# Optimization experiments

Measured on AMD Instinct MI355X. Metric: run time of the kernel, lower is better.

Reference implementation:

```python
import jax, jax.numpy as jnp
import numpy as np

IGNORE_INDEX = -100
VOCAB = 32000
D_MODEL = 2048


def setup_inputs() -> dict:
    key = jax.random.key(0)
    k1, k2, k3 = jax.random.split(key, 3)
    outputs = jax.random.normal(k1, (4, 2048, D_MODEL), dtype=jnp.float32)
    targets = jax.random.randint(k2, (4, 2048), 0, VOCAB, dtype=jnp.int64)
    # LM-head projection weight (torch nn.Linear stores [out_features, in_features]; no bias for LM heads)
    weight = jax.random.normal(k3, (VOCAB, D_MODEL), dtype=jnp.float32) * (D_MODEL ** -0.5)
    return {"outputs": outputs, "targets": targets, "weight": weight}


def reference(outputs, targets, weight):
    # Flatten tokens: [B, S, D] -> [N, D], [B, S] -> [N]
    d = outputs.shape[-1]
    hidden = outputs.reshape(-1, d)
    tgt = targets.reshape(-1)
    valid = tgt != IGNORE_INDEX
    safe_tgt = jnp.where(valid, tgt, 0)

    # Linear projection fused conceptually with CE; per-chunk sum-reduction CE
    # summed over chunks equals the full-batch sum, so we compute it vectorized.
    logits = jnp.einsum("nd,vd->nv", hidden, weight).astype(jnp.float32)  # [N, V]
    logp = jax.nn.log_softmax(logits, axis=-1)
    nll = -jnp.take_along_axis(logp, safe_tgt[:, None], axis=-1)[:, 0]  # [N]

    total_valid = jnp.sum(valid)
    total_loss = jnp.sum(jnp.where(valid, nll, 0.0))
    # forward returns 0.0 when no valid tokens; guard the division
    return jnp.where(total_valid > 0, total_loss / jnp.maximum(total_valid, 1).astype(total_loss.dtype), 0.0)
```

## Files before the change

### kernel.cpp

```cpp
#include <hip/hip_runtime.h>
#include <hip/hip_bf16.h>
#include <math.h>

#define D_MODEL 2048
#define VOCAB   32000
#define NTOK    8192
#define NCHUNK  (VOCAB / 64)

#define BM      128
#define BN      128
#define BK      32
#define LDK     (BK + 8)
#define MTILES  (NTOK / BM)
#define NTILES  (VOCAB / BN)

#define BM2     256
#define BN2     256
#define SUBK    64
#define NSUB    (D_MODEL / SUBK)
#define SUBSZ   32768
#define MT2     (NTOK / BM2)
#define NT2     (VOCAB / BN2)

typedef __attribute__((ext_vector_type(8))) short  frag8;
typedef __attribute__((ext_vector_type(4))) float  f32x4;
typedef __attribute__((ext_vector_type(4))) int    i32x4;
typedef __attribute__((ext_vector_type(8))) int    i32x8;


__device__ inline void g2l16(const void* g, void* l) {
    __builtin_amdgcn_global_load_lds(
        (const __attribute__((address_space(1))) unsigned int*)g,
        (__attribute__((address_space(3))) unsigned int*)l,
        16, 0, 0);
}

__device__ inline unsigned pack_bf16(float x, float y) {
    union { float f; unsigned u; } a, b;
    a.f = x; b.f = y;
    return __builtin_amdgcn_perm(b.u, a.u, 0x07060302u);
}


__global__ void cvt_fp8_kernel(const float* __restrict__ src, unsigned char* __restrict__ dst) {
    size_t i = (size_t)blockIdx.x * 256 + threadIdx.x;
    float4 v0 = ((const float4*)src)[2 * i];
    float4 v1 = ((const float4*)src)[2 * i + 1];
    int lo = 0, hi = 0;
    lo = __builtin_amdgcn_cvt_pk_fp8_f32(v0.x, v0.y, lo, 0);
    lo = __builtin_amdgcn_cvt_pk_fp8_f32(v0.z, v0.w, lo, 1);
    hi = __builtin_amdgcn_cvt_pk_fp8_f32(v1.x, v1.y, hi, 0);
    hi = __builtin_amdgcn_cvt_pk_fp8_f32(v1.z, v1.w, hi, 1);
    uint2 o = { (unsigned)lo, (unsigned)hi };
    ((uint2*)dst)[i] = o;
}


__global__ __launch_bounds__(512, 2)
void gemm_lse_fp8_v2(const unsigned char* __restrict__ Hq, const unsigned char* __restrict__ Wq,
                     float* __restrict__ partials) {
    extern __shared__ unsigned char lds[];

    const int L  = (blockIdx.x & 7) * 500 + (blockIdx.x >> 3);
    const int qs = L / 1000;
    const int rs = L % 1000;
    const int mtile = (rs & 7) + qs * 8;
    const int ntile = (rs >> 3) % 125;
    const int m0 = mtile * BM2;
    const int n0 = ntile * BN2;

    const int tid  = threadIdx.x;
    const int lane = tid & 63;
    const int w    = tid >> 6;
    const int wr   = w >> 2;
    const int wc   = w & 3;
    const int q    = lane >> 4;
    const int c    = lane & 15;

    const int sline = tid >> 3;
    const int sp    = (tid & 7) ^ (sline & 7);
    const int srow  = 2 * sline + (sp >> 2);
    const int sjj   = sp & 3;
    const unsigned char* gA = Hq + (size_t)(m0 + srow) * D_MODEL + sjj * 16;
    const unsigned char* gB = Wq + (size_t)(n0 + srow) * D_MODEL + sjj * 16;
    const unsigned wbase = (unsigned)w * 1024;

    const int prow = c >> 1;
    const int qh   = q >> 1;
    const int qb   = q & 1;
    const unsigned sA    = (unsigned)((((c & 1) << 2) | (qb << 1)) ^ prow) << 4;
    const unsigned aoff0 = (unsigned)(wr * 64 + prow) * 128 + sA;
    const unsigned aoff1 = aoff0 ^ 16;
    const unsigned boff0 = 16384u + (unsigned)(wc * 32 + prow) * 128 + sA;
    const unsigned boff1 = boff0 ^ 16;

    f32x4 acc[8][4];
    const f32x4 zero = {0.f, 0.f, 0.f, 0.f};
    #pragma unroll
    for (int i = 0; i < 8; ++i)
        #pragma unroll
        for (int j = 0; j < 4; ++j) acc[i][j] = zero;

    auto STAGE = [&](int s) {
        const unsigned base = (unsigned)(s & 3) * (unsigned)SUBSZ;
        const size_t ko = (size_t)s * SUBK;
        g2l16(gA + ko,                           lds + base + wbase);
        g2l16(gA + ko + (size_t)128 * D_MODEL,   lds + base + 8192 + wbase);
        g2l16(gB + ko,                           lds + base + 16384 + wbase);
        g2l16(gB + ko + (size_t)128 * D_MODEL,   lds + base + 24576 + wbase);
    };

    STAGE(0); STAGE(1); STAGE(2); STAGE(3);

    union Frag { i32x8 v; i32x4 h[2]; };

    #pragma unroll 1
    for (int t = 0; t < 16; ++t) {
        if (t == 15) asm volatile("s_waitcnt vmcnt(0)" ::: "memory");
        else         asm volatile("s_waitcnt vmcnt(8)" ::: "memory");
        __builtin_amdgcn_s_barrier();

        const unsigned ring   = (unsigned)(t & 1) * (2u * SUBSZ);
        const unsigned subsel = ring + (unsigned)qh * SUBSZ;
        const unsigned char* a0 = lds + subsel + aoff0;
        const unsigned char* a1 = lds + subsel + aoff1;
        const unsigned char* b0 = lds + subsel + boff0;
        const unsigned char* b1 = lds + subsel + boff1;

        i32x8 b8[4], fa, fb;

        #pragma unroll
        for (int ni = 0; ni < 4; ++ni) {
            Frag f;
            f.h[0] = *(const i32x4*)(b0 + ni * 1024);
            f.h[1] = *(const i32x4*)(b1 + ni * 1024);
            b8[ni] = f.v;
        }
        {
            Frag f0, f1;
            f0.h[0] = *(const i32x4*)(a0 + 0 * 1024);
            f0.h[1] = *(const i32x4*)(a1 + 0 * 1024);
            f1.h[0] = *(const i32x4*)(a0 + 1 * 1024);
            f1.h[1] = *(const i32x4*)(a1 + 1 * 1024);
            fa = f0.v; fb = f1.v;
        }
        asm volatile("s_waitcnt lgkmcnt(8)" ::: "memory");
        __builtin_amdgcn_s_barrier();
        asm volatile("s_waitcnt lgkmcnt(0)" ::: "memory");
        __builtin_amdgcn_sched_barrier(0);
        __builtin_amdgcn_s_setprio(1);
        #pragma unroll
        for (int ni = 0; ni < 4; ++ni)
            acc[0][ni] = __builtin_amdgcn_mfma_scale_f32_16x16x128_f8f6f4(
                fa, b8[ni], acc[0][ni], 0, 0, 0, 0x7F7F7F7F, 0, 0x7F7F7F7F);
        #pragma unroll
        for (int ni = 0; ni < 4; ++ni)
            acc[1][ni] = __builtin_amdgcn_mfma_scale_f32_16x16x128_f8f6f4(
                fb, b8[ni], acc[1][ni], 0, 0, 0, 0x7F7F7F7F, 0, 0x7F7F7F7F);
        __builtin_amdgcn_s_setprio(0);
        __builtin_amdgcn_s_barrier();

        #pragma unroll
        for (int p = 1; p < 3; ++p) {
            Frag f0, f1;
            f0.h[0] = *(const i32x4*)(a0 + (2 * p) * 1024);
            f0.h[1] = *(const i32x4*)(a1 + (2 * p) * 1024);
            f1.h[0] = *(const i32x4*)(a0 + (2 * p + 1) * 1024);
            f1.h[1] = *(const i32x4*)(a1 + (2 * p + 1) * 1024);
            fa = f0.v; fb = f1.v;
            __builtin_amdgcn_s_barrier();
            asm volatile("s_waitcnt lgkmcnt(0)" ::: "memory");
            __builtin_amdgcn_sched_barrier(0);
            __builtin_amdgcn_s_setprio(1);
            #pragma unroll
            for (int ni = 0; ni < 4; ++ni)
                acc[2 * p][ni] = __builtin_amdgcn_mfma_scale_f32_16x16x128_f8f6f4(
                    fa, b8[ni], acc[2 * p][ni], 0, 0, 0, 0x7F7F7F7F, 0, 0x7F7F7F7F);
            #pragma unroll
            for (int ni = 0; ni < 4; ++ni)
                acc[2 * p + 1][ni] = __builtin_amdgcn_mfma_scale_f32_16x16x128_f8f6f4(
                    fb, b8[ni], acc[2 * p + 1][ni], 0, 0, 0, 0x7F7F7F7F, 0, 0x7F7F7F7F);
            __builtin_amdgcn_s_setprio(0);
            __builtin_amdgcn_s_barrier();
        }

        {
            Frag f0, f1;
            f0.h[0] = *(const i32x4*)(a0 + 6 * 1024);
            f0.h[1] = *(const i32x4*)(a1 + 6 * 1024);
            f1.h[0] = *(const i32x4*)(a0 + 7 * 1024);
            f1.h[1] = *(const i32x4*)(a1 + 7 * 1024);
            fa = f0.v; fb = f1.v;
        }
        asm volatile("s_waitcnt lgkmcnt(0)" ::: "memory");
        __builtin_amdgcn_s_barrier();
        __builtin_amdgcn_sched_barrier(0);
        if (t < 14) { STAGE(2 * t + 4); STAGE(2 * t + 5); }
        __builtin_amdgcn_sched_barrier(0);
        __builtin_amdgcn_s_setprio(1);
        #pragma unroll
        for (int ni = 0; ni < 4; ++ni)
            acc[6][ni] = __builtin_amdgcn_mfma_scale_f32_16x16x128_f8f6f4(
                fa, b8[ni], acc[6][ni], 0, 0, 0, 0x7F7F7F7F, 0, 0x7F7F7F7F);
        #pragma unroll
        for (int ni = 0; ni < 4; ++ni)
            acc[7][ni] = __builtin_amdgcn_mfma_scale_f32_16x16x128_f8f6f4(
                fb, b8[ni], acc[7][ni], 0, 0, 0, 0x7F7F7F7F, 0, 0x7F7F7F7F);
        __builtin_amdgcn_s_setprio(0);
    }

    const int chunk = ntile * 4 + wc;
    #pragma unroll
    for (int mi = 0; mi < 8; ++mi) {
        #pragma unroll
        for (int r = 0; r < 4; ++r) {
            float v0 = acc[mi][0][r], v1 = acc[mi][1][r];
            float v2 = acc[mi][2][r], v3 = acc[mi][3][r];
            float mx = fmaxf(fmaxf(v0, v1), fmaxf(v2, v3));
            #pragma unroll
            for (int mask = 1; mask <= 8; mask <<= 1)
                mx = fmaxf(mx, __shfl_xor(mx, mask, 64));
            float sm = __expf(v0 - mx) + __expf(v1 - mx)
                     + __expf(v2 - mx) + __expf(v3 - mx);
            #pragma unroll
            for (int mask = 1; mask <= 8; mask <<= 1)
                sm += __shfl_xor(sm, mask, 64);
            if (c == 0) {
                int row_g = m0 + wr * 128 + mi * 16 + q * 4 + r;
                float* p = partials + ((size_t)row_g * NCHUNK + chunk) * 2;
                p[0] = mx;
                p[1] = sm;
            }
        }
    }
}


__global__ __launch_bounds__(256, 2)
void gemm_lse_f32(const float* __restrict__ H, const float* __restrict__ W,
                  float* __restrict__ partials) {
    __shared__ unsigned short As[BM][LDK];
    __shared__ unsigned short Bs[BN][LDK];

    const int GM = 8;
    int bid   = blockIdx.x;
    int super = bid / (GM * NTILES);
    int rem   = bid % (GM * NTILES);
    int mtile = super * GM + (rem % GM);
    int ntile = rem / GM;

    const int m0 = mtile * BM;
    const int n0 = ntile * BN;

    const int tid  = threadIdx.x;
    const int lane = tid & 63;
    const int w    = tid >> 6;
    const int wm   = (w >> 1) * 64;
    const int wn   = (w & 1)  * 64;
    const int q    = lane >> 4;
    const int c    = lane & 15;

    f32x4 acc[4][4];
    const f32x4 zero = {0.f, 0.f, 0.f, 0.f};
    #pragma unroll
    for (int i = 0; i < 4; ++i)
        #pragma unroll
        for (int j = 0; j < 4; ++j) acc[i][j] = zero;

    for (int kt = 0; kt < D_MODEL / BK; ++kt) {
        const int k0 = kt * BK;
        #pragma unroll
        for (int s = 0; s < 4; ++s) {
            int i   = tid + s * 256;
            int row = i >> 3;
            int kq  = (i & 7) << 2;

            const float4* pa = (const float4*)(H + (size_t)(m0 + row) * D_MODEL + k0 + kq);
            float4 va = *pa;
            uint2 ba = { pack_bf16(va.x, va.y), pack_bf16(va.z, va.w) };
            *(uint2*)&As[row][kq] = ba;

            const float4* pb = (const float4*)(W + (size_t)(n0 + row) * D_MODEL + k0 + kq);
            float4 vb = *pb;
            uint2 bb = { pack_bf16(vb.x, vb.y), pack_bf16(vb.z, vb.w) };
            *(uint2*)&Bs[row][kq] = bb;
        }
        __syncthreads();

        frag8 af[4], bf[4];
        #pragma unroll
        for (int t = 0; t < 4; ++t)
            af[t] = *(const frag8*)&As[wm + t * 16 + c][q * 8];
        #pragma unroll
        for (int t = 0; t < 4; ++t)
            bf[t] = *(const frag8*)&Bs[wn + t * 16 + c][q * 8];

        #pragma unroll
        for (int tm = 0; tm < 4; ++tm)
            #pragma unroll
            for (int tn = 0; tn < 4; ++tn)
                acc[tm][tn] = __builtin_amdgcn_mfma_f32_16x16x32_bf16(
                    af[tm], bf[tn], acc[tm][tn], 0, 0, 0);
        __syncthreads();
    }

    const int chunk = ntile * 2 + (w & 1);
    #pragma unroll
    for (int tm = 0; tm < 4; ++tm) {
        #pragma unroll
        for (int r = 0; r < 4; ++r) {
            float v0 = acc[tm][0][r], v1 = acc[tm][1][r];
            float v2 = acc[tm][2][r], v3 = acc[tm][3][r];
            float mx = fmaxf(fmaxf(v0, v1), fmaxf(v2, v3));
            #pragma unroll
            for (int mask = 1; mask <= 8; mask <<= 1)
                mx = fmaxf(mx, __shfl_xor(mx, mask, 64));
            float sm = __expf(v0 - mx) + __expf(v1 - mx)
                     + __expf(v2 - mx) + __expf(v3 - mx);
            #pragma unroll
            for (int mask = 1; mask <= 8; mask <<= 1)
                sm += __shfl_xor(sm, mask, 64);
            if (c == 0) {
                int row_g = m0 + wm + tm * 16 + q * 4 + r;
                float* p = partials + ((size_t)row_g * NCHUNK + chunk) * 2;
                p[0] = mx;
                p[1] = sm;
            }
        }
    }
}


__global__ __launch_bounds__(256)
void tgt_kernel(const float* __restrict__ H, const float* __restrict__ W,
                const int* __restrict__ targets, float* __restrict__ tgt_logit) {
    int token = blockIdx.x * 4 + (threadIdx.x >> 6);
    int lane  = threadIdx.x & 63;

    int t  = targets[token];
    int tt = (t == -100) ? 0 : t;
    const float4* h  = (const float4*)(H + (size_t)token * D_MODEL);
    const float4* wr = (const float4*)(W + (size_t)tt * D_MODEL);
    float p = 0.f;
    #pragma unroll
    for (int j = lane; j < D_MODEL / 4; j += 64) {
        float4 a = h[j], b = wr[j];
        p += a.x * b.x + a.y * b.y + a.z * b.z + a.w * b.w;
    }
    #pragma unroll
    for (int mask = 1; mask < 64; mask <<= 1)
        p += __shfl_xor(p, mask, 64);
    if (lane == 0) tgt_logit[token] = p;
}

__device__ inline void lse_merge(float& m, float& s, float om, float os) {
    if (om > m) { s = s * __expf(m - om) + os; m = om; }
    else        { s += os * __expf(om - m); }
}

__global__ __launch_bounds__(256)
void reduce_kernel(const float* __restrict__ partials,
                   const float* __restrict__ tgt_logit,
                   const int* __restrict__ targets,
                   float* __restrict__ nll) {
    int token = blockIdx.x * 4 + (threadIdx.x >> 6);
    int lane  = threadIdx.x & 63;

    float m = -INFINITY, s = 0.f;
    const float* base = partials + (size_t)token * NCHUNK * 2;
    for (int ch = lane; ch < NCHUNK; ch += 64) {
        float2 p = ((const float2*)base)[ch];
        lse_merge(m, s, p.x, p.y);
    }
    #pragma unroll
    for (int mask = 1; mask < 64; mask <<= 1) {
        float om = __shfl_xor(m, mask, 64);
        float os = __shfl_xor(s, mask, 64);
        lse_merge(m, s, om, os);
    }
    if (lane == 0) {
        int t = targets[token];
        nll[token] = (t != -100) ? (m + __logf(s) - tgt_logit[token]) : 0.0f;
    }
}

__global__ __launch_bounds__(256)
void final_kernel(const float* __restrict__ nll, const int* __restrict__ targets,
                  float* __restrict__ out) {
    int tid = threadIdx.x;
    float sum = 0.f, cnt = 0.f;
    for (int i = tid; i < NTOK; i += 256) {
        sum += nll[i];
        cnt += (targets[i] != -100) ? 1.0f : 0.0f;
    }
    #pragma unroll
    for (int mask = 1; mask < 64; mask <<= 1) {
        sum += __shfl_xor(sum, mask, 64);
        cnt += __shfl_xor(cnt, mask, 64);
    }
    __shared__ float lsum[4], lcnt[4];
    int lane = tid & 63, wid = tid >> 6;
    if (lane == 0) { lsum[wid] = sum; lcnt[wid] = cnt; }
    __syncthreads();
    if (tid == 0) {
        float S = lsum[0] + lsum[1] + lsum[2] + lsum[3];
        float C = lcnt[0] + lcnt[1] + lcnt[2] + lcnt[3];
        out[0] = (C > 0.f) ? (S / C) : 0.f;
    }
}


extern "C" void kernel_launch(void* const* d_in, const int* in_sizes, int n_in,
                              void* d_out, int out_size, void* d_ws, size_t ws_size,
                              hipStream_t stream) {
    (void)in_sizes; (void)n_in; (void)out_size;
    const float* H       = (const float*)d_in[0];
    const int*   targets = (const int*)d_in[1];
    const float* W       = (const float*)d_in[2];
    float*       out     = (float*)d_out;

    char* ws = (char*)d_ws;
    const size_t H8_BYTES   = (size_t)NTOK  * D_MODEL;
    const size_t W8_BYTES   = (size_t)VOCAB * D_MODEL;
    const size_t PART_BYTES = (size_t)NTOK * NCHUNK * 2 * 4;
    const size_t NEED = H8_BYTES + W8_BYTES + PART_BYTES + (size_t)NTOK * 8 + 64;

    if (ws_size >= NEED) {
        unsigned char* Hq = (unsigned char*)ws;
        unsigned char* Wq = (unsigned char*)(ws + H8_BYTES);
        float* partials   = (float*)(ws + H8_BYTES + W8_BYTES);
        float* tgt_logit  = (float*)(ws + H8_BYTES + W8_BYTES + PART_BYTES);
        float* nll        = tgt_logit + NTOK;

        static bool attr_done = false;
        if (!attr_done) {
            (void)hipFuncSetAttribute(reinterpret_cast<const void*>(gemm_lse_fp8_v2),
                                      hipFuncAttributeMaxDynamicSharedMemorySize, 131072);
            attr_done = true;
        }

        cvt_fp8_kernel<<<(NTOK  * D_MODEL / 8) / 256, 256, 0, stream>>>(H, Hq);
        cvt_fp8_kernel<<<(VOCAB * D_MODEL / 8) / 256, 256, 0, stream>>>(W, Wq);
        gemm_lse_fp8_v2<<<MT2 * NT2, 512, 131072, stream>>>(Hq, Wq, partials);
        tgt_kernel<<<NTOK / 4, 256, 0, stream>>>(H, W, targets, tgt_logit);
        reduce_kernel<<<NTOK / 4, 256, 0, stream>>>(partials, tgt_logit, targets, nll);
        final_kernel<<<1, 256, 0, stream>>>(nll, targets, out);
    } else {
        float* partials  = (float*)ws;
        float* tgt_logit = (float*)(ws + PART_BYTES);
        float* nll       = tgt_logit + NTOK;

        gemm_lse_f32<<<MTILES * NTILES, 256, 0, stream>>>(H, W, partials);
        tgt_kernel<<<NTOK / 4, 256, 0, stream>>>(H, W, targets, tgt_logit);
        reduce_kernel<<<NTOK / 4, 256, 0, stream>>>(partials, tgt_logit, targets, nll);
        final_kernel<<<1, 256, 0, stream>>>(nll, targets, out);
    }
}
```

Before: 1.171 ms.

## Double-buffer B fragments in registers across K iterations of FP8 GEMM

Restructures the main K loop so the B-operand fragments for the next ring are read from LDS into a second register set at the end of each iteration, alongside issuing the next global-to-LDS stages. The loop is unrolled by two to alternate the two register buffers, which removes the separate B-read and barrier phase at the top of each iteration. The goal is to hide LDS read latency behind the final MFMA block. In exchange it adds a full vmcnt(0) wait before staging, which shortens the global prefetch window, and it raises VGPR pressure with an extra set of B fragments.

```diff
diff --git a/kernel.cpp b/kernel.cpp
--- a/kernel.cpp
+++ b/kernel.cpp
@@ -101,73 +101,53 @@
         #pragma unroll
         for (int j = 0; j < 4; ++j) acc[i][j] = zero;
 
-    auto STAGE = [&](int s) {
-        const unsigned base = (unsigned)(s & 3) * (unsigned)SUBSZ;
-        const size_t ko = (size_t)s * SUBK;
-        g2l16(gA + ko,                           lds + base + wbase);
-        g2l16(gA + ko + (size_t)128 * D_MODEL,   lds + base + 8192 + wbase);
-        g2l16(gB + ko,                           lds + base + 16384 + wbase);
-        g2l16(gB + ko + (size_t)128 * D_MODEL,   lds + base + 24576 + wbase);
+    union Frag { i32x8 v; i32x4 h[2]; };
+
+    auto STAGE_AT = [&](size_t ko, unsigned slotbase) {
+        g2l16(gA + ko,                           lds + slotbase + wbase);
+        g2l16(gA + ko + (size_t)128 * D_MODEL,   lds + slotbase + 8192 + wbase);
+        g2l16(gB + ko,                           lds + slotbase + 16384 + wbase);
+        g2l16(gB + ko + (size_t)128 * D_MODEL,   lds + slotbase + 24576 + wbase);
     };
 
-    STAGE(0); STAGE(1); STAGE(2); STAGE(3);
-
-    union Frag { i32x8 v; i32x4 h[2]; };
-
-    #pragma unroll 1
-    for (int t = 0; t < 16; ++t) {
-        if (t == 15) asm volatile("s_waitcnt vmcnt(0)" ::: "memory");
-        else         asm volatile("s_waitcnt vmcnt(8)" ::: "memory");
-        __builtin_amdgcn_s_barrier();
-
-        const unsigned ring   = (unsigned)(t & 1) * (2u * SUBSZ);
-        const unsigned subsel = ring + (unsigned)qh * SUBSZ;
-        const unsigned char* a0 = lds + subsel + aoff0;
-        const unsigned char* a1 = lds + subsel + aoff1;
-        const unsigned char* b0 = lds + subsel + boff0;
-        const unsigned char* b1 = lds + subsel + boff1;
-
-        i32x8 b8[4], fa, fb;
-
+    auto READB = [&](unsigned pairbase, i32x8 (&dst)[4]) {
+        const unsigned char* b0 = lds + pairbase + (unsigned)qh * SUBSZ + boff0;
+        const unsigned char* b1 = lds + pairbase + (unsigned)qh * SUBSZ + boff1;
         #pragma unroll
         for (int ni = 0; ni < 4; ++ni) {
             Frag f;
             f.h[0] = *(const i32x4*)(b0 + ni * 1024);
             f.h[1] = *(const i32x4*)(b1 + ni * 1024);
-            b8[ni] = f.v;
-        }
-        {
-            Frag f0, f1;
-            f0.h[0] = *(const i32x4*)(a0 + 0 * 1024);
-            f0.h[1] = *(const i32x4*)(a1 + 0 * 1024);
-            f1.h[0] = *(const i32x4*)(a0 + 1 * 1024);
-            f1.h[1] = *(const i32x4*)(a1 + 1 * 1024);
-            fa = f0.v; fb = f1.v;
-        }
-        asm volatile("s_waitcnt lgkmcnt(8)" ::: "memory");
-        __builtin_amdgcn_s_barrier();
-        asm volatile("s_waitcnt lgkmcnt(0)" ::: "memory");
-        __builtin_amdgcn_sched_barrier(0);
-        __builtin_amdgcn_s_setprio(1);
-        #pragma unroll
-        for (int ni = 0; ni < 4; ++ni)
-            acc[0][ni] = __builtin_amdgcn_mfma_scale_f32_16x16x128_f8f6f4(
-                fa, b8[ni], acc[0][ni], 0, 0, 0, 0x7F7F7F7F, 0, 0x7F7F7F7F);
-        #pragma unroll
-        for (int ni = 0; ni < 4; ++ni)
-            acc[1][ni] = __builtin_amdgcn_mfma_scale_f32_16x16x128_f8f6f4(
-                fb, b8[ni], acc[1][ni], 0, 0, 0, 0x7F7F7F7F, 0, 0x7F7F7F7F);
-        __builtin_amdgcn_s_setprio(0);
-        __builtin_amdgcn_s_barrier();
-
-        #pragma unroll
-        for (int p = 1; p < 3; ++p) {
-            Frag f0, f1;
-            f0.h[0] = *(const i32x4*)(a0 + (2 * p) * 1024);
-            f0.h[1] = *(const i32x4*)(a1 + (2 * p) * 1024);
-            f1.h[0] = *(const i32x4*)(a0 + (2 * p + 1) * 1024);
-            f1.h[1] = *(const i32x4*)(a1 + (2 * p + 1) * 1024);
-            fa = f0.v; fb = f1.v;
+            dst[ni] = f.v;
+        }
+    };
+
+    i32x8 bA[4], bB[4];
+
+    STAGE_AT((size_t)0 * SUBK, 0);
+    STAGE_AT((size_t)1 * SUBK, SUBSZ);
+    STAGE_AT((size_t)2 * SUBK, 2 * SUBSZ);
+    STAGE_AT((size_t)3 * SUBK, 3 * SUBSZ);
+    asm volatile("s_waitcnt vmcnt(8)" ::: "memory");
+    __builtin_amdgcn_s_barrier();
+    READB(0, bA);
+
+    auto BODY = [&](int t, unsigned ring, i32x8 (&bcur)[4], i32x8 (&bnxt)[4],
+                    unsigned slotA, unsigned slotB) {
+        const unsigned char* a0 = lds + ring + (unsigned)qh * SUBSZ + aoff0;
+        const unsigned char* a1 = lds + ring + (unsigned)qh * SUBSZ + aoff1;
+        i32x8 fa, fb;
+
+        #pragma unroll
+        for (int p = 0; p < 3; ++p) {
+            {
+                Frag f0, f1;
+                f0.h[0] = *(const i32x4*)(a0 + (2 * p) * 1024);
+                f0.h[1] = *(const i32x4*)(a1 + (2 * p) * 1024);
+                f1.h[0] = *(const i32x4*)(a0 + (2 * p + 1) * 1024);
+                f1.h[1] = *(const i32x4*)(a1 + (2 * p + 1) * 1024);
+                fa = f0.v; fb = f1.v;
+            }
             __builtin_amdgcn_s_barrier();
             asm volatile("s_waitcnt lgkmcnt(0)" ::: "memory");
             __builtin_amdgcn_sched_barrier(0);
@@ -175,11 +155,11 @@
             #pragma unroll
             for (int ni = 0; ni < 4; ++ni)
                 acc[2 * p][ni] = __builtin_amdgcn_mfma_scale_f32_16x16x128_f8f6f4(
-                    fa, b8[ni], acc[2 * p][ni], 0, 0, 0, 0x7F7F7F7F, 0, 0x7F7F7F7F);
+                    fa, bcur[ni], acc[2 * p][ni], 0, 0, 0, 0x7F7F7F7F, 0, 0x7F7F7F7F);
             #pragma unroll
             for (int ni = 0; ni < 4; ++ni)
                 acc[2 * p + 1][ni] = __builtin_amdgcn_mfma_scale_f32_16x16x128_f8f6f4(
-                    fb, b8[ni], acc[2 * p + 1][ni], 0, 0, 0, 0x7F7F7F7F, 0, 0x7F7F7F7F);
+                    fb, bcur[ni], acc[2 * p + 1][ni], 0, 0, 0, 0x7F7F7F7F, 0, 0x7F7F7F7F);
             __builtin_amdgcn_s_setprio(0);
             __builtin_amdgcn_s_barrier();
         }
@@ -193,20 +173,31 @@
             fa = f0.v; fb = f1.v;
         }
         asm volatile("s_waitcnt lgkmcnt(0)" ::: "memory");
+        asm volatile("s_waitcnt vmcnt(0)" ::: "memory");
         __builtin_amdgcn_s_barrier();
         __builtin_amdgcn_sched_barrier(0);
-        if (t < 14) { STAGE(2 * t + 4); STAGE(2 * t + 5); }
+        if (t < 14) {
+            STAGE_AT((size_t)(2 * t + 4) * SUBK, slotA);
+            STAGE_AT((size_t)(2 * t + 5) * SUBK, slotB);
+        }
+        if (t < 15) READB(ring ^ (2u * SUBSZ), bnxt);
         __builtin_amdgcn_sched_barrier(0);
         __builtin_amdgcn_s_setprio(1);
         #pragma unroll
         for (int ni = 0; ni < 4; ++ni)
             acc[6][ni] = __builtin_amdgcn_mfma_scale_f32_16x16x128_f8f6f4(
-                fa, b8[ni], acc[6][ni], 0, 0, 0, 0x7F7F7F7F, 0, 0x7F7F7F7F);
+                fa, bcur[ni], acc[6][ni], 0, 0, 0, 0x7F7F7F7F, 0, 0x7F7F7F7F);
         #pragma unroll
         for (int ni = 0; ni < 4; ++ni)
             acc[7][ni] = __builtin_amdgcn_mfma_scale_f32_16x16x128_f8f6f4(
-                fb, b8[ni], acc[7][ni], 0, 0, 0, 0x7F7F7F7F, 0, 0x7F7F7F7F);
+                fb, bcur[ni], acc[7][ni], 0, 0, 0, 0x7F7F7F7F, 0, 0x7F7F7F7F);
         __builtin_amdgcn_s_setprio(0);
+    };
+
+    #pragma unroll 1
+    for (int t2 = 0; t2 < 8; ++t2) {
+        BODY(2 * t2,     0,           bA, bB, 0,           SUBSZ);
+        BODY(2 * t2 + 1, 2u * SUBSZ,  bB, bA, 2u * SUBSZ,  3u * SUBSZ);
     }
 
     const int chunk = ntile * 4 + wc;
```

After: 4.298 ms. +267.0%, slower.
